# Kernel optimization log

Hardware: AMD Instinct MI355X
Metric: run time of the kernel (lower is better)

The kernel has to match this reference:

```python
import jax, jax.numpy as jnp
import numpy as np

LAMADA = 0.0001
USER_NUM, ITEM_NUM, FACTOR = 100000, 50000, 64
N_EDGES, BATCH = 3200000, 4096


def setup_inputs() -> dict:
    key = jax.random.key(0)
    ks = jax.random.split(key, 11)
    return {
        "embed_user": jax.random.normal(ks[0], (USER_NUM, FACTOR), jnp.float32) * 0.01,
        "embed_item": jax.random.normal(ks[1], (ITEM_NUM, FACTOR), jnp.float32) * 0.01,
        "u_idx": jax.random.randint(ks[2], (N_EDGES,), 0, USER_NUM, jnp.int32),
        "i_idx": jax.random.randint(ks[3], (N_EDGES,), 0, ITEM_NUM, jnp.int32),
        "ui_vals": jax.random.uniform(ks[4], (N_EDGES,), jnp.float32),
        "iu_vals": jax.random.uniform(ks[5], (N_EDGES,), jnp.float32),
        "d_i": jax.random.uniform(ks[6], (USER_NUM,), jnp.float32),
        "d_j": jax.random.uniform(ks[7], (ITEM_NUM,), jnp.float32),
        "user": jax.random.randint(ks[8], (BATCH,), 0, USER_NUM, jnp.int32),
        "item_i": jax.random.randint(ks[9], (BATCH,), 0, ITEM_NUM, jnp.int32),
        "item_j": jax.random.randint(ks[10], (BATCH,), 0, ITEM_NUM, jnp.int32),
    }


def _spmm_u(i_emb, u_idx, i_idx, vals):
    # user_item_matrix @ items_embedding  (COO SpMM via segment_sum)
    msg = i_emb[i_idx] * vals[:, None]  # [E, F]
    return jax.ops.segment_sum(msg, u_idx, num_segments=USER_NUM)


def _spmm_i(u_emb, u_idx, i_idx, vals):
    # item_user_matrix @ users_embedding
    msg = u_emb[u_idx] * vals[:, None]  # [E, F]
    return jax.ops.segment_sum(msg, i_idx, num_segments=ITEM_NUM)


def reference(embed_user, embed_item, u_idx, i_idx, ui_vals, iu_vals,
              d_i, d_j, user, item_i, item_j):
    di = d_i[:, None]  # [U,1] broadcast == expand(-1, factor_num)
    dj = d_j[:, None]  # [I,1]

    gcn1_u = _spmm_u(embed_item, u_idx, i_idx, ui_vals) + embed_user * di
    gcn1_i = _spmm_i(embed_user, u_idx, i_idx, iu_vals) + embed_item * dj
    gcn2_u = _spmm_u(gcn1_i, u_idx, i_idx, ui_vals) + gcn1_u * di
    gcn2_i = _spmm_i(gcn1_u, u_idx, i_idx, iu_vals) + gcn1_i * dj

    gcn_u = embed_user + gcn1_u + gcn2_u
    gcn_i = embed_item + gcn1_i + gcn2_i

    u = gcn_u[user]        # [B, F]
    pi = gcn_i[item_i]     # [B, F]
    pj = gcn_i[item_j]     # [B, F]

    pred_i = jnp.sum(u * pi, axis=-1)
    pred_j = jnp.sum(u * pj, axis=-1)

    l2 = LAMADA * jnp.mean(u ** 2) + LAMADA * jnp.mean(pi ** 2 + pj ** 2)
    # -log(sigmoid(x)) == softplus(-x), numerically stable
    loss2 = jnp.mean(jax.nn.softplus(-(pred_i - pred_j)))
    return loss2 + l2
```

## Files before the change

kernel.cpp:

```cpp
#include <hip/hip_runtime.h>
#include <math.h>

#define USER_NUM 100000
#define ITEM_NUM 50000
#define FACTOR   64
#define LAMADA   0.0001f

#define RB_BITS 7
#define RB      128
#define NBU   782
#define NBI   391
#define CAPU  5120
#define CAPI  9216
#define CHUNK 8192

#define FP8_SCALE    256.0f
#define FP8_INVSCALE 0.00390625f

typedef unsigned short ushort_t;
typedef unsigned int   uint_t;
typedef float v2f_t __attribute__((ext_vector_type(2)));

__device__ __forceinline__ void dec8(uint2 t, float* __restrict__ f) {
    v2f_t p0 = __builtin_amdgcn_cvt_pk_f32_fp8(t.x, false);
    v2f_t p1 = __builtin_amdgcn_cvt_pk_f32_fp8(t.x, true);
    v2f_t p2 = __builtin_amdgcn_cvt_pk_f32_fp8(t.y, false);
    v2f_t p3 = __builtin_amdgcn_cvt_pk_f32_fp8(t.y, true);
    f[0] = p0.x; f[1] = p0.y; f[2] = p1.x; f[3] = p1.y;
    f[4] = p2.x; f[5] = p2.y; f[6] = p3.x; f[7] = p3.y;
}
__device__ __forceinline__ uint_t enc1(float v) {
    return (uint_t)__builtin_amdgcn_cvt_pk_fp8_f32(v, v, 0, false) & 0xFFu;
}
__device__ __forceinline__ float decv(uint_t e) {
    v2f_t p = __builtin_amdgcn_cvt_pk_f32_fp8(e, false);
    return p.x;
}

__device__ __forceinline__ void acc8p(uint2 t, float v, v2f_t* __restrict__ S) {
    v2f_t vv = {v, v};
    S[0] = __builtin_elementwise_fma(vv, __builtin_amdgcn_cvt_pk_f32_fp8(t.x, false), S[0]);
    S[1] = __builtin_elementwise_fma(vv, __builtin_amdgcn_cvt_pk_f32_fp8(t.x, true),  S[1]);
    S[2] = __builtin_elementwise_fma(vv, __builtin_amdgcn_cvt_pk_f32_fp8(t.y, false), S[2]);
    S[3] = __builtin_elementwise_fma(vv, __builtin_amdgcn_cvt_pk_f32_fp8(t.y, true),  S[3]);
}

__global__ void to_fp8_both(const float* __restrict__ a, int n4a,
                            const float* __restrict__ b, int n4b,
                            unsigned char* __restrict__ da, unsigned char* __restrict__ db) {
    int gid = blockIdx.x * blockDim.x + threadIdx.x;
    const float* src; unsigned char* dst; int idx;
    if (gid < n4a) { src = a; dst = da; idx = gid; }
    else if (gid < n4a + n4b) { src = b; dst = db; idx = gid - n4a; }
    else return;
    float4 v = ((const float4*)src)[idx];
    int r = __builtin_amdgcn_cvt_pk_fp8_f32(v.x * FP8_SCALE, v.y * FP8_SCALE, 0, false);
    r = __builtin_amdgcn_cvt_pk_fp8_f32(v.z * FP8_SCALE, v.w * FP8_SCALE, r, true);
    ((uint_t*)dst)[idx] = (uint_t)r;
}

__global__ void init_cursors(int* __restrict__ cur_u, int* __restrict__ cur_i) {
    int t = blockIdx.x * blockDim.x + threadIdx.x;
    if (t < NBU) cur_u[t] = t * CAPU;
    if (t < NBI) cur_i[t] = t * CAPI;
}

__global__ void place(const int* __restrict__ u_idx, const int* __restrict__ i_idx,
                      const float* __restrict__ ui_vals, const float* __restrict__ iu_vals,
                      int* __restrict__ cur_u, int* __restrict__ cur_i,
                      uint_t* __restrict__ staged_u, uint_t* __restrict__ staged_i, int n_edges) {
    __shared__ int s_u[NBU];
    __shared__ int s_i[NBI];
    int tid = threadIdx.x;
    for (int b = tid; b < NBU; b += 1024) s_u[b] = 0;
    for (int b = tid; b < NBI; b += 1024) s_i[b] = 0;
    __syncthreads();
    int start = blockIdx.x * CHUNK, end = min(start + CHUNK, n_edges);
    int len = end - start;
    int vend = start + (len & ~1023);
    for (int e4 = start + tid * 4; e4 < vend; e4 += 4096) {
        int4 uu = *(const int4*)(u_idx + e4);
        int4 ii = *(const int4*)(i_idx + e4);
        atomicAdd(&s_u[uu.x >> RB_BITS], 1); atomicAdd(&s_u[uu.y >> RB_BITS], 1);
        atomicAdd(&s_u[uu.z >> RB_BITS], 1); atomicAdd(&s_u[uu.w >> RB_BITS], 1);
        atomicAdd(&s_i[ii.x >> RB_BITS], 1); atomicAdd(&s_i[ii.y >> RB_BITS], 1);
        atomicAdd(&s_i[ii.z >> RB_BITS], 1); atomicAdd(&s_i[ii.w >> RB_BITS], 1);
    }
    for (int e = vend + tid; e < end; e += 1024) {
        atomicAdd(&s_u[u_idx[e] >> RB_BITS], 1);
        atomicAdd(&s_i[i_idx[e] >> RB_BITS], 1);
    }
    __syncthreads();
    for (int b = tid; b < NBU; b += 1024) { int c = s_u[b]; s_u[b] = c ? atomicAdd(&cur_u[b], c) : 0; }
    for (int b = tid; b < NBI; b += 1024) { int c = s_i[b]; s_i[b] = c ? atomicAdd(&cur_i[b], c) : 0; }
    __syncthreads();
    for (int e4 = start + tid * 4; e4 < vend; e4 += 4096) {
        int4 uu = *(const int4*)(u_idx + e4);
        int4 ii = *(const int4*)(i_idx + e4);
        float4 uv = *(const float4*)(ui_vals + e4);
        float4 iv = *(const float4*)(iu_vals + e4);
        int pu0 = atomicAdd(&s_u[uu.x >> RB_BITS], 1);
        int pu1 = atomicAdd(&s_u[uu.y >> RB_BITS], 1);
        int pu2 = atomicAdd(&s_u[uu.z >> RB_BITS], 1);
        int pu3 = atomicAdd(&s_u[uu.w >> RB_BITS], 1);
        int pi0 = atomicAdd(&s_i[ii.x >> RB_BITS], 1);
        int pi1 = atomicAdd(&s_i[ii.y >> RB_BITS], 1);
        int pi2 = atomicAdd(&s_i[ii.z >> RB_BITS], 1);
        int pi3 = atomicAdd(&s_i[ii.w >> RB_BITS], 1);
        staged_u[pu0] = ((uint_t)(uu.x & (RB-1)) << 25) | ((uint_t)ii.x << 8) | enc1(uv.x);
        staged_u[pu1] = ((uint_t)(uu.y & (RB-1)) << 25) | ((uint_t)ii.y << 8) | enc1(uv.y);
        staged_u[pu2] = ((uint_t)(uu.z & (RB-1)) << 25) | ((uint_t)ii.z << 8) | enc1(uv.z);
        staged_u[pu3] = ((uint_t)(uu.w & (RB-1)) << 25) | ((uint_t)ii.w << 8) | enc1(uv.w);
        staged_i[pi0] = ((uint_t)(ii.x & (RB-1)) << 25) | ((uint_t)uu.x << 8) | enc1(iv.x);
        staged_i[pi1] = ((uint_t)(ii.y & (RB-1)) << 25) | ((uint_t)uu.y << 8) | enc1(iv.y);
        staged_i[pi2] = ((uint_t)(ii.z & (RB-1)) << 25) | ((uint_t)uu.z << 8) | enc1(iv.z);
        staged_i[pi3] = ((uint_t)(ii.w & (RB-1)) << 25) | ((uint_t)uu.w << 8) | enc1(iv.w);
    }
    for (int e = vend + tid; e < end; e += 1024) {
        int u = u_idx[e], i = i_idx[e];
        int pu = atomicAdd(&s_u[u >> RB_BITS], 1);
        staged_u[pu] = ((uint_t)(u & (RB-1)) << 25) | ((uint_t)i << 8) | enc1(ui_vals[e]);
        int pi = atomicAdd(&s_i[i >> RB_BITS], 1);
        staged_i[pi] = ((uint_t)(i & (RB-1)) << 25) | ((uint_t)u << 8) | enc1(iu_vals[e]);
    }
}

__global__ void bucket_finalize(const uint_t* __restrict__ staged, const int* __restrict__ cur,
                                int cap, int* __restrict__ ptr, uint_t* __restrict__ cs,
                                int n_rows) {
    __shared__ int s_cnt[RB];
    __shared__ int s_pos[RB];
    int b = blockIdx.x, tid = threadIdx.x;
    int sbase = b * cap;
    int nE = cur[b] - sbase;
    if (tid < RB) s_cnt[tid] = 0;
    __syncthreads();
    int nE8 = nE & ~7;
    for (int k = tid * 8; k < nE8; k += 2048) {
        uint4 a = *(const uint4*)(staged + sbase + k);
        uint4 c = *(const uint4*)(staged + sbase + k + 4);
        atomicAdd(&s_cnt[a.x >> 25], 1); atomicAdd(&s_cnt[a.y >> 25], 1);
        atomicAdd(&s_cnt[a.z >> 25], 1); atomicAdd(&s_cnt[a.w >> 25], 1);
        atomicAdd(&s_cnt[c.x >> 25], 1); atomicAdd(&s_cnt[c.y >> 25], 1);
        atomicAdd(&s_cnt[c.z >> 25], 1); atomicAdd(&s_cnt[c.w >> 25], 1);
    }
    if (tid == 0) for (int k = nE8; k < nE; ++k) atomicAdd(&s_cnt[staged[sbase + k] >> 25], 1);
    __syncthreads();
    int x = (tid < RB) ? s_cnt[tid] : 0;
    if (tid < RB) s_pos[tid] = x;
    __syncthreads();
    for (int off = 1; off < RB; off <<= 1) {
        int t = (tid < RB && tid >= off) ? s_pos[tid - off] : 0;
        __syncthreads();
        if (tid < RB) s_pos[tid] += t;
        __syncthreads();
    }
    if (tid < RB) {
        int excl = s_pos[tid] - x + sbase;
        int r = (b << RB_BITS) + tid;
        if (r < n_rows) ptr[r + b] = excl;
        s_pos[tid] = excl;
    }
    if (tid == 0) ptr[min((b << RB_BITS) + RB, n_rows) + b] = sbase + nE;
    __syncthreads();
    for (int k = tid * 8; k < nE8; k += 2048) {
        uint4 a = *(const uint4*)(staged + sbase + k);
        uint4 c = *(const uint4*)(staged + sbase + k + 4);
        int p0 = atomicAdd(&s_pos[a.x >> 25], 1);
        int p1 = atomicAdd(&s_pos[a.y >> 25], 1);
        int p2 = atomicAdd(&s_pos[a.z >> 25], 1);
        int p3 = atomicAdd(&s_pos[a.w >> 25], 1);
        int p4 = atomicAdd(&s_pos[c.x >> 25], 1);
        int p5 = atomicAdd(&s_pos[c.y >> 25], 1);
        int p6 = atomicAdd(&s_pos[c.z >> 25], 1);
        int p7 = atomicAdd(&s_pos[c.w >> 25], 1);
        cs[p0] = a.x & 0x01FFFFFFu; cs[p1] = a.y & 0x01FFFFFFu;
        cs[p2] = a.z & 0x01FFFFFFu; cs[p3] = a.w & 0x01FFFFFFu;
        cs[p4] = c.x & 0x01FFFFFFu; cs[p5] = c.y & 0x01FFFFFFu;
        cs[p6] = c.z & 0x01FFFFFFu; cs[p7] = c.w & 0x01FFFFFFu;
    }
    if (tid == 0) for (int k = nE8; k < nE; ++k) {
        uint_t se = staged[sbase + k];
        int pos = atomicAdd(&s_pos[se >> 25], 1);
        cs[pos] = se & 0x01FFFFFFu;
    }
}

__device__ __forceinline__ void gather_dot8f8(const uint_t* __restrict__ cs, int start, int end,
                                              const uint2* __restrict__ tab2, int g, int l,
                                              float* __restrict__ acc) {
    v2f_t A[4] = {{0.f,0.f},{0.f,0.f},{0.f,0.f},{0.f,0.f}};
    v2f_t B[4] = {{0.f,0.f},{0.f,0.f},{0.f,0.f},{0.f,0.f}};
    const uint2* __restrict__ tl = tab2 + l;
    int k = start;
    for (; k + 32 <= end; k += 32) {
        uint_t c0 = cs[k + g];
        uint_t c1 = cs[k + 8 + g];
        uint_t c2 = cs[k + 16 + g];
        uint_t c3 = cs[k + 24 + g];
        uint2 t0 = tl[(c0 >> 8) << 3];
        uint2 t1 = tl[(c1 >> 8) << 3];
        uint2 t2 = tl[(c2 >> 8) << 3];
        uint2 t3 = tl[(c3 >> 8) << 3];
        float v0 = decv(c0);
        float v1 = decv(c1);
        float v2 = decv(c2);
        float v3 = decv(c3);
        acc8p(t0, v0, A);
        acc8p(t1, v1, B);
        acc8p(t2, v2, A);
        acc8p(t3, v3, B);
    }
    if (k + 16 <= end) {
        uint_t c0 = cs[k + g];
        uint_t c1 = cs[k + 8 + g];
        uint2 t0 = tl[(c0 >> 8) << 3];
        uint2 t1 = tl[(c1 >> 8) << 3];
        acc8p(t0, decv(c0), A);
        acc8p(t1, decv(c1), B);
        k += 16;
    }
    if (k + 8 <= end) {
        uint_t c0 = cs[k + g];
        uint2 t0 = tl[(c0 >> 8) << 3];
        acc8p(t0, decv(c0), A);
        k += 8;
    }
    if (k + g < end) {
        uint_t c0 = cs[k + g];
        uint2 t0 = tl[(c0 >> 8) << 3];
        acc8p(t0, decv(c0), B);
    }
    #pragma unroll
    for (int i = 0; i < 4; ++i) {
        v2f_t s = A[i] + B[i];
        float r0 = s.x, r1 = s.y;
        r0 += __shfl_xor(r0, 8, 64);
        r1 += __shfl_xor(r1, 8, 64);
        r0 += __shfl_xor(r0, 16, 64);
        r1 += __shfl_xor(r1, 16, 64);
        r0 += __shfl_xor(r0, 32, 64);
        r1 += __shfl_xor(r1, 32, 64);
        acc[2 * i]     = r0;
        acc[2 * i + 1] = r1;
    }
}

__global__ void csr_spmm5(const int* __restrict__ ptr_u, const uint_t* __restrict__ cs_u,
                          const int* __restrict__ ptr_i, const uint_t* __restrict__ cs_i,
                          const uint2* __restrict__ beu2, const uint2* __restrict__ bei2,
                          const float* __restrict__ eu, const float* __restrict__ ei,
                          const float* __restrict__ d_i, const float* __restrict__ d_j,
                          uint2* __restrict__ g1u2, uint2* __restrict__ g1i2) {
    int w = (blockIdx.x * blockDim.x + threadIdx.x) >> 6;
    int lane = threadIdx.x & 63;
    int g = lane >> 3, l = lane & 7;
    const int* ptr; const uint_t* cs; const uint2* src; const float* self;
    const float* d; uint2* out; int row;
    if (w < USER_NUM) {
        row = w; ptr = ptr_u; cs = cs_u; src = bei2; self = eu; d = d_i; out = g1u2;
    } else if (w < USER_NUM + ITEM_NUM) {
        row = w - USER_NUM; ptr = ptr_i; cs = cs_i; src = beu2; self = ei; d = d_j; out = g1i2;
    } else return;
    int pidx = row + (row >> RB_BITS);
    int start = ptr[pidx], end = ptr[pidx + 1];
    float acc[8];
    gather_dot8f8(cs, start, end, src, g, l, acc);
    if (g == 0) {
        float4 s0 = ((const float4*)self)[(size_t)row * 16 + l * 2];
        float4 s1 = ((const float4*)self)[(size_t)row * 16 + l * 2 + 1];
        float dv = d[row] * FP8_SCALE;
        float o0 = acc[0] + s0.x * dv, o1 = acc[1] + s0.y * dv;
        float o2 = acc[2] + s0.z * dv, o3 = acc[3] + s0.w * dv;
        float o4 = acc[4] + s1.x * dv, o5 = acc[5] + s1.y * dv;
        float o6 = acc[6] + s1.z * dv, o7 = acc[7] + s1.w * dv;
        int r0 = __builtin_amdgcn_cvt_pk_fp8_f32(o0, o1, 0, false);
        r0 = __builtin_amdgcn_cvt_pk_fp8_f32(o2, o3, r0, true);
        int r1 = __builtin_amdgcn_cvt_pk_fp8_f32(o4, o5, 0, false);
        r1 = __builtin_amdgcn_cvt_pk_fp8_f32(o6, o7, r1, true);
        uint2 o; o.x = (uint_t)r0; o.y = (uint_t)r1;
        out[(size_t)row * 8 + l] = o;
    }
}

__global__ void gather_rows(const float* __restrict__ eu, const float* __restrict__ ei,
                            const uint2* __restrict__ g1u2, const uint2* __restrict__ g1i2,
                            const int* __restrict__ ptr_u, const uint_t* __restrict__ cs_u,
                            const int* __restrict__ ptr_i, const uint_t* __restrict__ cs_i,
                            const float* __restrict__ d_i, const float* __restrict__ d_j,
                            const int* __restrict__ user, const int* __restrict__ item_i,
                            const int* __restrict__ item_j, float* __restrict__ rows, int batch) {
    int w = (blockIdx.x * blockDim.x + threadIdx.x) >> 6;
    int lane = threadIdx.x & 63;
    int g = lane >> 3, l = lane & 7;
    if (w >= 3 * batch) return;
    int role = w / batch;
    int s = w - role * batch;
    int row; const int* ptr; const uint_t* cs; const uint2* tab; const uint2* g1t;
    const float* self; float sc;
    if (role == 0) {
        row = user[s]; ptr = ptr_u; cs = cs_u; tab = g1i2; g1t = g1u2;
        self = eu; sc = 1.f + d_i[row];
    } else {
        row = (role == 1) ? item_i[s] : item_j[s];
        ptr = ptr_i; cs = cs_i; tab = g1u2; g1t = g1i2;
        self = ei; sc = 1.f + d_j[row];
    }
    int pidx = row + (row >> RB_BITS);
    float acc[8];
    gather_dot8f8(cs, ptr[pidx], ptr[pidx + 1], tab, g, l, acc);
    if (g == 0) {
        uint2 gg = g1t[(size_t)row * 8 + l];
        float gf[8];
        dec8(gg, gf);
        float4 e0 = ((const float4*)self)[(size_t)row * 16 + l * 2];
        float4 e1 = ((const float4*)self)[(size_t)row * 16 + l * 2 + 1];
        float4 o0, o1;
        o0.x = e0.x + (gf[0] * sc + acc[0]) * FP8_INVSCALE;
        o0.y = e0.y + (gf[1] * sc + acc[1]) * FP8_INVSCALE;
        o0.z = e0.z + (gf[2] * sc + acc[2]) * FP8_INVSCALE;
        o0.w = e0.w + (gf[3] * sc + acc[3]) * FP8_INVSCALE;
        o1.x = e1.x + (gf[4] * sc + acc[4]) * FP8_INVSCALE;
        o1.y = e1.y + (gf[5] * sc + acc[5]) * FP8_INVSCALE;
        o1.z = e1.z + (gf[6] * sc + acc[6]) * FP8_INVSCALE;
        o1.w = e1.w + (gf[7] * sc + acc[7]) * FP8_INVSCALE;
        ((float4*)rows)[(size_t)w * 16 + l * 2]     = o0;
        ((float4*)rows)[(size_t)w * 16 + l * 2 + 1] = o1;
    }
}

__global__ void loss_dots(const float* __restrict__ rows, float* __restrict__ partials,
                          int batch, int nblocks) {
    __shared__ float s_su2[4], s_sp2[4], s_sp[4];
    int w = (blockIdx.x * blockDim.x + threadIdx.x) >> 6;
    int lane = threadIdx.x & 63;
    int wid = (threadIdx.x >> 6);
    float su2 = 0.f, sp2 = 0.f, sp = 0.f;
    if (w < batch) {
        float U  = rows[(size_t)w * FACTOR + lane];
        float Pi = rows[(size_t)(batch + w) * FACTOR + lane];
        float Pj = rows[(size_t)(2 * batch + w) * FACTOR + lane];
        float di  = U * Pi;
        float dj  = U * Pj;
        su2 = U * U;
        sp2 = Pi * Pi + Pj * Pj;
        for (int off = 32; off; off >>= 1) {
            di  += __shfl_down(di,  off, 64);
            dj  += __shfl_down(dj,  off, 64);
            su2 += __shfl_down(su2, off, 64);
            sp2 += __shfl_down(sp2, off, 64);
        }
        if (lane == 0) {
            float x = -(di - dj);
            sp = fmaxf(x, 0.f) + log1pf(expf(-fabsf(x)));
        }
    }
    if (lane == 0) { s_su2[wid] = su2; s_sp2[wid] = sp2; s_sp[wid] = sp; }
    __syncthreads();
    if (threadIdx.x == 0) {
        int b = blockIdx.x;
        partials[b]               = s_su2[0] + s_su2[1] + s_su2[2] + s_su2[3];
        partials[nblocks + b]     = s_sp2[0] + s_sp2[1] + s_sp2[2] + s_sp2[3];
        partials[2 * nblocks + b] = s_sp[0]  + s_sp[1]  + s_sp[2]  + s_sp[3];
    }
}

__global__ void reduce_partials(const float* __restrict__ partials, int nblocks,
                                float* __restrict__ out, int batch) {
    __shared__ float s0[1024], s1[1024], s2[1024];
    int tid = threadIdx.x;
    float a = 0.f, b = 0.f, c = 0.f;
    for (int k = tid; k < nblocks; k += 1024) {
        a += partials[k];
        b += partials[nblocks + k];
        c += partials[2 * nblocks + k];
    }
    s0[tid] = a; s1[tid] = b; s2[tid] = c;
    __syncthreads();
    for (int off = 512; off; off >>= 1) {
        if (tid < off) {
            s0[tid] += s0[tid + off];
            s1[tid] += s1[tid + off];
            s2[tid] += s2[tid + off];
        }
        __syncthreads();
    }
    if (tid == 0) {
        float inv_b  = 1.0f / (float)batch;
        float inv_bf = 1.0f / (float)(batch * FACTOR);
        out[0] = s2[0] * inv_b + LAMADA * s0[0] * inv_bf + LAMADA * s1[0] * inv_bf;
    }
}

__global__ void init_scale(const float* __restrict__ src, const float* __restrict__ d,
                           float* __restrict__ dst, int n_rows) {
    int gid = blockIdx.x * blockDim.x + threadIdx.x;
    int total = n_rows * 16;
    if (gid >= total) return;
    int r = gid >> 4;
    float s = d[r];
    float4 v = ((const float4*)src)[gid];
    v.x *= s; v.y *= s; v.z *= s; v.w *= s;
    ((float4*)dst)[gid] = v;
}

__global__ void edge_spmm(const float* __restrict__ srcU, const float* __restrict__ srcI,
                          float* __restrict__ dstU, float* __restrict__ dstI,
                          const int* __restrict__ u_idx, const int* __restrict__ i_idx,
                          const float* __restrict__ ui_vals, const float* __restrict__ iu_vals,
                          int n_edges) {
    long long gid = (long long)blockIdx.x * blockDim.x + threadIdx.x;
    int e = (int)(gid >> 4);
    if (e >= n_edges) return;
    int sub = ((int)gid & 15) * 4;
    int u = u_idx[e], i = i_idx[e];
    float uv = ui_vals[e], iv = iu_vals[e];
    size_t uo = (size_t)u * FACTOR + sub;
    size_t io = (size_t)i * FACTOR + sub;
    float4 a = *(const float4*)(srcI + io);
    float4 b = *(const float4*)(srcU + uo);
    float* du = dstU + uo;
    float* di = dstI + io;
    atomicAdd(du + 0, a.x * uv); atomicAdd(du + 1, a.y * uv);
    atomicAdd(du + 2, a.z * uv); atomicAdd(du + 3, a.w * uv);
    atomicAdd(di + 0, b.x * iv); atomicAdd(di + 1, b.y * iv);
    atomicAdd(di + 2, b.z * iv); atomicAdd(di + 3, b.w * iv);
}

__global__ void batch_loss(const float* __restrict__ eu, const float* __restrict__ ei,
                           const float* __restrict__ g1u, const float* __restrict__ g1i,
                           const float* __restrict__ g2u, const float* __restrict__ g2i,
                           const int* __restrict__ user, const int* __restrict__ item_i,
                           const int* __restrict__ item_j, float* __restrict__ acc, int batch) {
    int gid = blockIdx.x * blockDim.x + threadIdx.x;
    int w = gid >> 6;
    int lane = threadIdx.x & 63;
    if (w >= batch) return;
    int uu = user[w], ii = item_i[w], jj = item_j[w];
    size_t uo = (size_t)uu * FACTOR + lane;
    size_t io = (size_t)ii * FACTOR + lane;
    size_t jo = (size_t)jj * FACTOR + lane;
    float uvv = eu[uo] + g1u[uo] + g2u[uo];
    float piv = ei[io] + g1i[io] + g2i[io];
    float pjv = ei[jo] + g1i[jo] + g2i[jo];
    float di  = uvv * piv;
    float dj  = uvv * pjv;
    float su2 = uvv * uvv;
    float sp2 = piv * piv + pjv * pjv;
    for (int off = 32; off; off >>= 1) {
        di  += __shfl_down(di,  off, 64);
        dj  += __shfl_down(dj,  off, 64);
        su2 += __shfl_down(su2, off, 64);
        sp2 += __shfl_down(sp2, off, 64);
    }
    if (lane == 0) {
        float x  = -(di - dj);
        float sp = fmaxf(x, 0.f) + log1pf(expf(-fabsf(x)));
        atomicAdd(acc + 0, su2);
        atomicAdd(acc + 1, sp2);
        atomicAdd(acc + 2, sp);
    }
}

__global__ void finalize_fb(const float* __restrict__ acc, float* __restrict__ out, int batch) {
    if (threadIdx.x == 0 && blockIdx.x == 0) {
        float inv_b  = 1.0f / (float)batch;
        float inv_bf = 1.0f / (float)(batch * FACTOR);
        out[0] = acc[2] * inv_b + LAMADA * acc[0] * inv_bf + LAMADA * acc[1] * inv_bf;
    }
}

extern "C" void kernel_launch(void* const* d_in, const int* in_sizes, int n_in,
                              void* d_out, int out_size, void* d_ws, size_t ws_size,
                              hipStream_t stream) {
    const float* eu      = (const float*)d_in[0];
    const float* ei      = (const float*)d_in[1];
    const int*   u_idx   = (const int*)d_in[2];
    const int*   i_idx   = (const int*)d_in[3];
    const float* ui_vals = (const float*)d_in[4];
    const float* iu_vals = (const float*)d_in[5];
    const float* d_i     = (const float*)d_in[6];
    const float* d_j     = (const float*)d_in[7];
    const int*   user    = (const int*)d_in[8];
    const int*   item_i  = (const int*)d_in[9];
    const int*   item_j  = (const int*)d_in[10];
    int n_edges = in_sizes[2];
    int batch   = in_sizes[8];
    float* out  = (float*)d_out;

    const size_t FU = (size_t)USER_NUM * FACTOR;
    const size_t FI = (size_t)ITEM_NUM * FACTOR;
    const size_t CU_SZ = (size_t)NBU * CAPU;
    const size_t CI_SZ = (size_t)NBI * CAPI;

    const size_t APAD_BYTES = (FU + FI) * 2;
    unsigned char* g1u8 = (unsigned char*)d_ws;
    unsigned char* g1i8 = g1u8 + FU;
    unsigned char* beu8 = g1i8 + FI;
    unsigned char* bei8 = beu8 + FU;
    uint_t* cs_u  = (uint_t*)((char*)d_ws + APAD_BYTES);
    uint_t* cs_i  = cs_u + CU_SZ;
    uint_t* staged_u = (uint_t*)d_ws;
    uint_t* staged_i = cs_u;
    int*   ptr_u = (int*)(cs_i + CI_SZ);
    int*   ptr_i = ptr_u + (USER_NUM + NBU + 2);
    int*   cur_u = ptr_i + (ITEM_NUM + NBI + 2);
    int*   cur_i = cur_u + NBU;
    float* rows  = (float*)(cur_i + NBI);
    int    nblk_loss = (batch * 64 + 255) / 256;
    float* partials = rows + (size_t)3 * batch * FACTOR;

    size_t need_bytes = ((size_t)(partials + (size_t)3 * nblk_loss) - (size_t)d_ws);

    if (ws_size >= need_bytes) {
        int nb1 = (n_edges + CHUNK - 1) / CHUNK;

        init_cursors<<<(NBU + 255) / 256, 256, 0, stream>>>(cur_u, cur_i);
        place<<<nb1, 1024, 0, stream>>>(u_idx, i_idx, ui_vals, iu_vals,
                                        cur_u, cur_i, staged_u, staged_i, n_edges);
        bucket_finalize<<<NBI, 256, 0, stream>>>(staged_i, cur_i, CAPI, ptr_i, cs_i, ITEM_NUM);
        bucket_finalize<<<NBU, 256, 0, stream>>>(staged_u, cur_u, CAPU, ptr_u, cs_u, USER_NUM);

        int n4u = (int)(FU / 4), n4i = (int)(FI / 4);
        to_fp8_both<<<(n4u + n4i + 255) / 256, 256, 0, stream>>>(eu, n4u, ei, n4i, beu8, bei8);

        int total_waves = USER_NUM + ITEM_NUM;
        csr_spmm5<<<(total_waves * 64 + 255) / 256, 256, 0, stream>>>(
            ptr_u, cs_u, ptr_i, cs_i, (const uint2*)beu8, (const uint2*)bei8,
            eu, ei, d_i, d_j, (uint2*)g1u8, (uint2*)g1i8);

        gather_rows<<<(3 * batch * 64 + 255) / 256, 256, 0, stream>>>(
            eu, ei, (const uint2*)g1u8, (const uint2*)g1i8,
            ptr_u, cs_u, ptr_i, cs_i, d_i, d_j, user, item_i, item_j, rows, batch);
        loss_dots<<<nblk_loss, 256, 0, stream>>>(rows, partials, batch, nblk_loss);
        reduce_partials<<<1, 1024, 0, stream>>>(partials, nblk_loss, out, batch);
    } else {
        float* f_g1u = (float*)d_ws;
        float* f_g1i = f_g1u + FU;
        float* f_g2u = f_g1i + FI;
        float* f_g2i = f_g2u + FU;
        float* f_acc = f_g2i + FI;
        hipMemsetAsync(f_acc, 0, 4 * sizeof(float), stream);
        long long tot = (long long)n_edges * 16;
        int eblocks = (int)((tot + 255) / 256);
        init_scale<<<(USER_NUM * 16 + 255) / 256, 256, 0, stream>>>(eu, d_i, f_g1u, USER_NUM);
        init_scale<<<(ITEM_NUM * 16 + 255) / 256, 256, 0, stream>>>(ei, d_j, f_g1i, ITEM_NUM);
        edge_spmm<<<eblocks, 256, 0, stream>>>(eu, ei, f_g1u, f_g1i, u_idx, i_idx, ui_vals, iu_vals, n_edges);
        init_scale<<<(USER_NUM * 16 + 255) / 256, 256, 0, stream>>>(f_g1u, d_i, f_g2u, USER_NUM);
        init_scale<<<(ITEM_NUM * 16 + 255) / 256, 256, 0, stream>>>(f_g1i, d_j, f_g2i, ITEM_NUM);
        edge_spmm<<<eblocks, 256, 0, stream>>>(f_g1u, f_g1i, f_g2u, f_g2i, u_idx, i_idx, ui_vals, iu_vals, n_edges);
        batch_loss<<<(batch * 64 + 255) / 256, 256, 0, stream>>>(eu, ei, f_g1u, f_g1i, f_g2u, f_g2i,
                                                                 user, item_i, item_j, f_acc, batch);
        finalize_fb<<<1, 64, 0, stream>>>(f_acc, out, batch);
    }
}
```

Measured before the change: 345.3 us.

## Stage bucketed edges in shared memory before coalesced global scatter

The edge placement kernel now handles the user and item directions as two separate phases. Each phase counts the chunk's edges per bucket, takes a block-wide prefix scan, and writes the packed edges into a shared-memory staging buffer in bucket order. Those buffers are then copied to global memory in contiguous runs per bucket, with a binary search finding each element's bucket. This replaces the random per-edge global stores with mostly coalesced writes, at the cost of extra barriers, a 1024-wide scan, and 32KB+ of LDS per block, which reduces occupancy.

```diff
diff --git a/kernel.cpp b/kernel.cpp
--- a/kernel.cpp
+++ b/kernel.cpp
@@ -65,64 +65,92 @@
     if (t < NBI) cur_i[t] = t * CAPI;
 }
 
-__global__ void place(const int* __restrict__ u_idx, const int* __restrict__ i_idx,
-                      const float* __restrict__ ui_vals, const float* __restrict__ iu_vals,
-                      int* __restrict__ cur_u, int* __restrict__ cur_i,
-                      uint_t* __restrict__ staged_u, uint_t* __restrict__ staged_i, int n_edges) {
-    __shared__ int s_u[NBU];
-    __shared__ int s_i[NBI];
+__device__ __forceinline__ void place_phase(
+    const int* __restrict__ rows_idx, const int* __restrict__ cols_idx,
+    const float* __restrict__ vals, int* __restrict__ cur,
+    uint_t* __restrict__ staged, int nb, int start, int end,
+    uint_t* __restrict__ s_stage, int* __restrict__ s_cnt,
+    int* __restrict__ s_scan, int* __restrict__ s_gbase) {
     int tid = threadIdx.x;
-    for (int b = tid; b < NBU; b += 1024) s_u[b] = 0;
-    for (int b = tid; b < NBI; b += 1024) s_i[b] = 0;
-    __syncthreads();
-    int start = blockIdx.x * CHUNK, end = min(start + CHUNK, n_edges);
     int len = end - start;
-    int vend = start + (len & ~1023);
-    for (int e4 = start + tid * 4; e4 < vend; e4 += 4096) {
-        int4 uu = *(const int4*)(u_idx + e4);
-        int4 ii = *(const int4*)(i_idx + e4);
-        atomicAdd(&s_u[uu.x >> RB_BITS], 1); atomicAdd(&s_u[uu.y >> RB_BITS], 1);
-        atomicAdd(&s_u[uu.z >> RB_BITS], 1); atomicAdd(&s_u[uu.w >> RB_BITS], 1);
-        atomicAdd(&s_i[ii.x >> RB_BITS], 1); atomicAdd(&s_i[ii.y >> RB_BITS], 1);
-        atomicAdd(&s_i[ii.z >> RB_BITS], 1); atomicAdd(&s_i[ii.w >> RB_BITS], 1);
+    s_cnt[tid] = 0;
+    __syncthreads();
+    int vend = start + (len & ~3);
+    for (int e = start + tid * 4; e < vend; e += 4096) {
+        int4 r = *(const int4*)(rows_idx + e);
+        atomicAdd(&s_cnt[r.x >> RB_BITS], 1);
+        atomicAdd(&s_cnt[r.y >> RB_BITS], 1);
+        atomicAdd(&s_cnt[r.z >> RB_BITS], 1);
+        atomicAdd(&s_cnt[r.w >> RB_BITS], 1);
     }
     for (int e = vend + tid; e < end; e += 1024) {
-        atomicAdd(&s_u[u_idx[e] >> RB_BITS], 1);
-        atomicAdd(&s_i[i_idx[e] >> RB_BITS], 1);
-    }
-    __syncthreads();
-    for (int b = tid; b < NBU; b += 1024) { int c = s_u[b]; s_u[b] = c ? atomicAdd(&cur_u[b], c) : 0; }
-    for (int b = tid; b < NBI; b += 1024) { int c = s_i[b]; s_i[b] = c ? atomicAdd(&cur_i[b], c) : 0; }
-    __syncthreads();
-    for (int e4 = start + tid * 4; e4 < vend; e4 += 4096) {
-        int4 uu = *(const int4*)(u_idx + e4);
-        int4 ii = *(const int4*)(i_idx + e4);
-        float4 uv = *(const float4*)(ui_vals + e4);
-        float4 iv = *(const float4*)(iu_vals + e4);
-        int pu0 = atomicAdd(&s_u[uu.x >> RB_BITS], 1);
-        int pu1 = atomicAdd(&s_u[uu.y >> RB_BITS], 1);
-        int pu2 = atomicAdd(&s_u[uu.z >> RB_BITS], 1);
-        int pu3 = atomicAdd(&s_u[uu.w >> RB_BITS], 1);
-        int pi0 = atomicAdd(&s_i[ii.x >> RB_BITS], 1);
-        int pi1 = atomicAdd(&s_i[ii.y >> RB_BITS], 1);
-        int pi2 = atomicAdd(&s_i[ii.z >> RB_BITS], 1);
-        int pi3 = atomicAdd(&s_i[ii.w >> RB_BITS], 1);
-        staged_u[pu0] = ((uint_t)(uu.x & (RB-1)) << 25) | ((uint_t)ii.x << 8) | enc1(uv.x);
-        staged_u[pu1] = ((uint_t)(uu.y & (RB-1)) << 25) | ((uint_t)ii.y << 8) | enc1(uv.y);
-        staged_u[pu2] = ((uint_t)(uu.z & (RB-1)) << 25) | ((uint_t)ii.z << 8) | enc1(uv.z);
-        staged_u[pu3] = ((uint_t)(uu.w & (RB-1)) << 25) | ((uint_t)ii.w << 8) | enc1(uv.w);
-        staged_i[pi0] = ((uint_t)(ii.x & (RB-1)) << 25) | ((uint_t)uu.x << 8) | enc1(iv.x);
-        staged_i[pi1] = ((uint_t)(ii.y & (RB-1)) << 25) | ((uint_t)uu.y << 8) | enc1(iv.y);
-        staged_i[pi2] = ((uint_t)(ii.z & (RB-1)) << 25) | ((uint_t)uu.z << 8) | enc1(iv.z);
-        staged_i[pi3] = ((uint_t)(ii.w & (RB-1)) << 25) | ((uint_t)uu.w << 8) | enc1(iv.w);
+        atomicAdd(&s_cnt[rows_idx[e] >> RB_BITS], 1);
+    }
+    __syncthreads();
+    int c = s_cnt[tid];
+    s_scan[tid] = c;
+    __syncthreads();
+    #pragma unroll
+    for (int off = 1; off < 1024; off <<= 1) {
+        int v = (tid >= off) ? s_scan[tid - off] : 0;
+        __syncthreads();
+        s_scan[tid] += v;
+        __syncthreads();
+    }
+    int excl = s_scan[tid] - c;
+    __syncthreads();
+    s_scan[tid] = excl;
+    if (tid < nb) {
+        s_gbase[tid] = c ? atomicAdd(&cur[tid], c) : 0;
+        s_cnt[tid] = excl;
+    }
+    __syncthreads();
+    for (int e = start + tid * 4; e < vend; e += 4096) {
+        int4 r = *(const int4*)(rows_idx + e);
+        int4 cc = *(const int4*)(cols_idx + e);
+        float4 v = *(const float4*)(vals + e);
+        int p0 = atomicAdd(&s_cnt[r.x >> RB_BITS], 1);
+        int p1 = atomicAdd(&s_cnt[r.y >> RB_BITS], 1);
+        int p2 = atomicAdd(&s_cnt[r.z >> RB_BITS], 1);
+        int p3 = atomicAdd(&s_cnt[r.w >> RB_BITS], 1);
+        s_stage[p0] = ((uint_t)(r.x & (RB-1)) << 25) | ((uint_t)cc.x << 8) | enc1(v.x);
+        s_stage[p1] = ((uint_t)(r.y & (RB-1)) << 25) | ((uint_t)cc.y << 8) | enc1(v.y);
+        s_stage[p2] = ((uint_t)(r.z & (RB-1)) << 25) | ((uint_t)cc.z << 8) | enc1(v.z);
+        s_stage[p3] = ((uint_t)(r.w & (RB-1)) << 25) | ((uint_t)cc.w << 8) | enc1(v.w);
     }
     for (int e = vend + tid; e < end; e += 1024) {
-        int u = u_idx[e], i = i_idx[e];
-        int pu = atomicAdd(&s_u[u >> RB_BITS], 1);
-        staged_u[pu] = ((uint_t)(u & (RB-1)) << 25) | ((uint_t)i << 8) | enc1(ui_vals[e]);
-        int pi = atomicAdd(&s_i[i >> RB_BITS], 1);
-        staged_i[pi] = ((uint_t)(i & (RB-1)) << 25) | ((uint_t)u << 8) | enc1(iu_vals[e]);
-    }
+        int rr = rows_idx[e];
+        int p = atomicAdd(&s_cnt[rr >> RB_BITS], 1);
+        s_stage[p] = ((uint_t)(rr & (RB-1)) << 25) | ((uint_t)cols_idx[e] << 8) | enc1(vals[e]);
+    }
+    __syncthreads();
+    for (int t = tid; t < len; t += 1024) {
+        int lo = 0, hi = nb;
+        while (hi - lo > 1) {
+            int mid = (lo + hi) >> 1;
+            if (s_scan[mid] <= t) lo = mid; else hi = mid;
+        }
+        staged[s_gbase[lo] + (t - s_scan[lo])] = s_stage[t];
+    }
+    __syncthreads();
+}
+
+__global__ __launch_bounds__(1024) void place2(
+        const int* __restrict__ u_idx, const int* __restrict__ i_idx,
+        const float* __restrict__ ui_vals, const float* __restrict__ iu_vals,
+        int* __restrict__ cur_u, int* __restrict__ cur_i,
+        uint_t* __restrict__ staged_u, uint_t* __restrict__ staged_i, int n_edges) {
+    __shared__ uint_t s_stage[CHUNK];
+    __shared__ int s_cnt[1024];
+    __shared__ int s_scan[1025];
+    __shared__ int s_gbase[1024];
+    int start = blockIdx.x * CHUNK;
+    int end = min(start + CHUNK, n_edges);
+    if (start >= end) return;
+    place_phase(u_idx, i_idx, ui_vals, cur_u, staged_u, NBU, start, end,
+                s_stage, s_cnt, s_scan, s_gbase);
+    place_phase(i_idx, u_idx, iu_vals, cur_i, staged_i, NBI, start, end,
+                s_stage, s_cnt, s_scan, s_gbase);
 }
 
 __global__ void bucket_finalize(const uint_t* __restrict__ staged, const int* __restrict__ cur,
@@ -516,8 +544,8 @@
         int nb1 = (n_edges + CHUNK - 1) / CHUNK;
 
         init_cursors<<<(NBU + 255) / 256, 256, 0, stream>>>(cur_u, cur_i);
-        place<<<nb1, 1024, 0, stream>>>(u_idx, i_idx, ui_vals, iu_vals,
-                                        cur_u, cur_i, staged_u, staged_i, n_edges);
+        place2<<<nb1, 1024, 0, stream>>>(u_idx, i_idx, ui_vals, iu_vals,
+                                         cur_u, cur_i, staged_u, staged_i, n_edges);
         bucket_finalize<<<NBI, 256, 0, stream>>>(staged_i, cur_i, CAPI, ptr_i, cs_i, ITEM_NUM);
         bucket_finalize<<<NBU, 256, 0, stream>>>(staged_u, cur_u, CAPU, ptr_u, cs_u, USER_NUM);
 
```

New measurement: 311.9 us. 9.7% less time.
